# Kernel tuning notes

Measured on AMD Instinct MI355X. Metric: run time of the kernel, lower is better.

The kernel has to match this reference:

```python
import jax, jax.numpy as jnp
import numpy as np

N = 100_000   # active voxels
CIN = 64
COUT = 64
K = 3
L = 128       # voxel grid extent per axis
C = K // 2    # kernel center


def _offsets():
    # spatial offsets (z, y, x) for all non-center kernel taps, in the same
    # enumeration order as the original module's triple loop
    offs = []
    for dz in range(K):
        for dy in range(K):
            for dx in range(K):
                if (dz, dy, dx) != (C, C, C):
                    offs.append((dz - C, dy - C, dx - C))
    return offs


def _build_neighbor_map(coords):
    # coords: [N,3] int, unique. For each offset build (out_idx, in_idx) pairs
    # where voxel out_idx has an active neighbor in_idx at coords+offset.
    keys = (coords[:, 0].astype(np.int64) * L + coords[:, 1]) * L + coords[:, 2]
    order = np.argsort(keys)
    skeys = keys[order]
    pairs = []
    for (z, y, x) in _offsets():
        nb = coords + np.array([z, y, x], dtype=coords.dtype)
        valid = np.all((nb >= 0) & (nb < L), axis=1)
        nkeys = (nb[:, 0].astype(np.int64) * L + nb[:, 1]) * L + nb[:, 2]
        pos = np.clip(np.searchsorted(skeys, nkeys), 0, N - 1)
        found = valid & (skeys[pos] == nkeys)
        out_idx = np.nonzero(found)[0].astype(np.int32)
        in_idx = order[pos[found]].astype(np.int32)
        pairs.append((out_idx, in_idx))
    P = max(len(o) for o, _ in pairs)
    nei = np.zeros((len(pairs), P, 2), dtype=np.int32)
    sizes = np.zeros(len(pairs), dtype=np.int32)
    for i, (o, j) in enumerate(pairs):
        nei[i, :len(o), 0] = o
        nei[i, :len(o), 1] = j
        sizes[i] = len(o)
    return nei, sizes


def setup_inputs() -> dict:
    rng = np.random.default_rng(0)
    flat = rng.choice(L * L * L, size=N, replace=False)  # unique voxel coords
    coords = np.stack([flat // (L * L), (flat // L) % L, flat % L], axis=1).astype(np.int32)
    nei, sizes = _build_neighbor_map(coords)
    key = jax.random.key(0)
    k1, k2, k3 = jax.random.split(key, 3)
    sp_values = jax.random.normal(k1, (N, CIN), dtype=jnp.float32)
    weight = jax.random.normal(k2, (COUT, K, K, K, CIN), dtype=jnp.float32) * 0.05
    bias = jax.random.normal(k3, (COUT,), dtype=jnp.float32)
    return {"sp_values": sp_values, "weight": weight, "bias": bias,
            "nei_indices": jnp.asarray(nei), "nei_sizes": jnp.asarray(sizes)}


def reference(sp_values, weight, bias, nei_indices, nei_sizes):
    # weight: [Cout,kz,ky,kx,Cin] -> [kz,ky,kx,Cin,Cout] (matches torch permute)
    w = jnp.transpose(weight, (1, 2, 3, 4, 0))
    out = sp_values @ w[C, C, C]                                   # center tap: [N,Cout]
    offs = _offsets()
    w_offs = jnp.stack([w[z + C, y + C, x + C] for (z, y, x) in offs])  # [O,Cin,Cout]
    P = nei_indices.shape[1]
    valid = (jnp.arange(P)[None, :] < nei_sizes[:, None]).astype(sp_values.dtype)  # [O,P]
    gathered = sp_values[nei_indices[:, :, 1]] * valid[:, :, None]  # [O,P,Cin], padded rows zeroed
    contrib = jnp.einsum('opc,ocd->opd', gathered, w_offs)          # [O,P,Cout]
    out = out.at[nei_indices[:, :, 0].reshape(-1)].add(contrib.reshape(-1, out.shape[1]))
    return out + bias
```

## Files before the change

kernel.cpp:

```cpp
#include <hip/hip_runtime.h>


typedef __bf16 bf16x8 __attribute__((ext_vector_type(8)));
typedef float f32x4 __attribute__((ext_vector_type(4)));

#define LDSP 72

__device__ __forceinline__ unsigned short f2bf(float f) {
    union { float f; unsigned int u; } v; v.f = f;
    unsigned int u = v.u;
    return (unsigned short)((u + 0x7FFFu + ((u >> 16) & 1u)) >> 16);
}

__device__ __forceinline__ ushort4 cvt4(float4 v) {
    ushort4 b;
    b.x = f2bf(v.x); b.y = f2bf(v.y); b.z = f2bf(v.z); b.w = f2bf(v.w);
    return b;
}

__global__ __launch_bounds__(256) void sp3d_prep(
    const float* __restrict__ sp, const float* __restrict__ w,
    unsigned short* __restrict__ spb, unsigned short* __restrict__ wb,
    int* __restrict__ tbl, int n_rows)
{
    const long gt = (long)blockIdx.x * 256 + threadIdx.x;
    const long stride = (long)gridDim.x * 256;

    const long ntbl = 26L * n_rows;
    for (long i = gt; i < (ntbl >> 2); i += stride)
        *(int4*)&tbl[i * 4] = make_int4(-1, -1, -1, -1);
    if (gt < (ntbl & 3)) tbl[(ntbl & ~3L) + gt] = -1;

    const long nsp = (long)n_rows * 16;
    for (long i = gt; i < nsp; i += stride) {
        float4 v = *(const float4*)&sp[i * 4];
        *(ushort4*)&spb[i * 4] = cvt4(v);
    }

    for (long i = gt; i < 27 * 1024; i += stride) {
        int tp = (int)(i >> 10);
        int r  = (int)(i & 1023);
        int n = r >> 4, k4 = r & 15;
        float4 v = *(const float4*)&w[n * 1728 + tp * 64 + k4 * 4];
        *(ushort4*)&wb[(tp * 64 + n) * 64 + k4 * 4] = cvt4(v);
    }
}

__global__ __launch_bounds__(256) void sp3d_build(
    const int* __restrict__ nei, const int* __restrict__ sizes,
    int* __restrict__ tbl, int n_rows, int P)
{
    const int o = blockIdx.y;
    const int p = blockIdx.x * 256 + threadIdx.x;
    if (p < sizes[o]) {
        int2 pr = *(const int2*)&nei[(o * P + p) * 2];
        tbl[(long)o * n_rows + pr.x] = pr.y;
    }
}

__global__ __launch_bounds__(256) void sp3d_main(
    const unsigned short* __restrict__ spb, const unsigned short* __restrict__ wb,
    const float* __restrict__ bias, const int* __restrict__ tbl,
    float* __restrict__ out, int n_rows)
{
    __shared__ unsigned short Bt[2][64 * LDSP];
    __shared__ int tl[26][256];

    const int t = threadIdx.x;
    const int row0 = blockIdx.x * 256;
    const int wid = t >> 6, lane = t & 63, ml = lane & 15, quad = lane >> 4;

    {
        int r = row0 + t;
        if (r >= n_rows) r = n_rows - 1;
        #pragma unroll
        for (int o = 0; o < 26; ++o)
            tl[o][t] = tbl[(long)o * n_rows + r];
    }
    {
        int c = t;
        *(bf16x8*)&Bt[0][(c >> 3) * LDSP + (c & 7) * 8] = *(const bf16x8*)(wb + c * 8);
        c = t + 256;
        *(bf16x8*)&Bt[0][(c >> 3) * LDSP + (c & 7) * 8] = *(const bf16x8*)(wb + c * 8);
    }

    f32x4 acc[4][4];
    #pragma unroll
    for (int mg = 0; mg < 4; ++mg)
        #pragma unroll
        for (int nt = 0; nt < 4; ++nt) acc[mg][nt] = f32x4{0.f, 0.f, 0.f, 0.f};

    __syncthreads();

    int cur = 0;
    for (int tp = 0; tp < 27; ++tp) {
        bf16x8 b0[4], b1[4];
        #pragma unroll
        for (int nt = 0; nt < 4; ++nt) {
            b0[nt] = *(const bf16x8*)&Bt[cur][(nt * 16 + ml) * LDSP + quad * 8];
            b1[nt] = *(const bf16x8*)&Bt[cur][(nt * 16 + ml) * LDSP + 32 + quad * 8];
        }

        bf16x8 s0, s1;
        if (tp < 26) {
            const unsigned short* src = wb + (tp + 1) * 4096;
            s0 = *(const bf16x8*)(src + t * 8);
            s1 = *(const bf16x8*)(src + (t + 256) * 8);
        }

        int inr[4];
        #pragma unroll
        for (int mg = 0; mg < 4; ++mg) {
            int rl = wid * 64 + mg * 16 + ml;
            if (tp == 13) {
                int r = row0 + rl;
                inr[mg] = (r < n_rows) ? r : n_rows - 1;
            } else {
                int o = tp - (tp > 13 ? 1 : 0);
                inr[mg] = tl[o][rl];
            }
        }

        #pragma unroll
        for (int mg = 0; mg < 4; ++mg) {
            if (__any(inr[mg] >= 0)) {
                bf16x8 a0, a1;
                #pragma unroll
                for (int j = 0; j < 8; ++j) { a0[j] = (__bf16)0.f; a1[j] = (__bf16)0.f; }
                if (inr[mg] >= 0) {
                    const unsigned short* ap = spb + (long)inr[mg] * 64 + quad * 8;
                    a0 = *(const bf16x8*)ap;
                    a1 = *(const bf16x8*)(ap + 32);
                }
                #pragma unroll
                for (int nt = 0; nt < 4; ++nt) {
                    acc[mg][nt] = __builtin_amdgcn_mfma_f32_16x16x32_bf16(a0, b0[nt], acc[mg][nt], 0, 0, 0);
                    acc[mg][nt] = __builtin_amdgcn_mfma_f32_16x16x32_bf16(a1, b1[nt], acc[mg][nt], 0, 0, 0);
                }
            }
        }

        if (tp < 26) {
            int c = t;
            *(bf16x8*)&Bt[cur ^ 1][(c >> 3) * LDSP + (c & 7) * 8] = s0;
            c = t + 256;
            *(bf16x8*)&Bt[cur ^ 1][(c >> 3) * LDSP + (c & 7) * 8] = s1;
        }
        __syncthreads();
        cur ^= 1;
    }

    float bv[4];
    #pragma unroll
    for (int nt = 0; nt < 4; ++nt) bv[nt] = bias[nt * 16 + ml];
    #pragma unroll
    for (int mg = 0; mg < 4; ++mg) {
        int rb = row0 + wid * 64 + mg * 16 + quad * 4;
        #pragma unroll
        for (int nt = 0; nt < 4; ++nt) {
            int col = nt * 16 + ml;
            #pragma unroll
            for (int rg = 0; rg < 4; ++rg) {
                int row = rb + rg;
                if (row < n_rows) out[(long)row * 64 + col] = acc[mg][nt][rg] + bv[nt];
            }
        }
    }
}

extern "C" void kernel_launch(void* const* d_in, const int* in_sizes, int n_in,
                              void* d_out, int out_size, void* d_ws, size_t ws_size,
                              hipStream_t stream) {
    const float* sp    = (const float*)d_in[0];
    const float* w     = (const float*)d_in[1];
    const float* bias  = (const float*)d_in[2];
    const int*   nei   = (const int*)d_in[3];
    const int*   sizes = (const int*)d_in[4];
    float* out = (float*)d_out;

    const int N = in_sizes[0] / 64;
    const int P = in_sizes[3] / (26 * 2);

    char* ws = (char*)d_ws;
    unsigned short* spb = (unsigned short*)ws;
    size_t off = ((size_t)N * 64 * 2 + 255) & ~(size_t)255;
    unsigned short* wb = (unsigned short*)(ws + off);
    off = (off + 27 * 64 * 64 * 2 + 255) & ~(size_t)255;
    int* tbl = (int*)(ws + off);

    sp3d_prep<<<dim3(1024), 256, 0, stream>>>(sp, w, spb, wb, tbl, N);
    sp3d_build<<<dim3((P + 255) / 256, 26), 256, 0, stream>>>(nei, sizes, tbl, N, P);
    sp3d_main<<<dim3((N + 255) / 256), 256, 0, stream>>>(spb, wb, bias, tbl, out, N);
}
```

Before: 140.3 us.

## Prefetch next-tap gathered rows and pre-swizzle weights into MFMA fragment layout

Result: faster. 133.0 us (-5.3%).

```diff
diff --git a/kernel.cpp b/kernel.cpp
--- a/kernel.cpp
+++ b/kernel.cpp
@@ -3,8 +3,6 @@
 
 typedef __bf16 bf16x8 __attribute__((ext_vector_type(8)));
 typedef float f32x4 __attribute__((ext_vector_type(4)));
-
-#define LDSP 72
 
 __device__ __forceinline__ unsigned short f2bf(float f) {
     union { float f; unsigned int u; } v; v.f = f;
@@ -37,12 +35,16 @@
         *(ushort4*)&spb[i * 4] = cvt4(v);
     }
 
-    for (long i = gt; i < 27 * 1024; i += stride) {
-        int tp = (int)(i >> 10);
-        int r  = (int)(i & 1023);
-        int n = r >> 4, k4 = r & 15;
-        float4 v = *(const float4*)&w[n * 1728 + tp * 64 + k4 * 4];
-        *(ushort4*)&wb[(tp * 64 + n) * 64 + k4 * 4] = cvt4(v);
+    for (long i = gt; i < 27 * 512; i += stride) {
+        int tap = (int)(i >> 9);
+        int rem = (int)(i & 511);
+        int fragid = rem >> 6, lane = rem & 63;
+        int nt = fragid >> 1, half = fragid & 1, ml = lane & 15, quad = lane >> 4;
+        const float* src = w + (nt * 16 + ml) * 1728 + tap * 64 + half * 32 + quad * 8;
+        float4 v0 = *(const float4*)src;
+        float4 v1 = *(const float4*)(src + 4);
+        *(ushort4*)&wb[i * 8]     = cvt4(v0);
+        *(ushort4*)&wb[i * 8 + 4] = cvt4(v1);
     }
 }
 
@@ -58,112 +60,90 @@
     }
 }
 
-__global__ __launch_bounds__(256) void sp3d_main(
+__global__ __launch_bounds__(512) void sp3d_main(
     const unsigned short* __restrict__ spb, const unsigned short* __restrict__ wb,
     const float* __restrict__ bias, const int* __restrict__ tbl,
     float* __restrict__ out, int n_rows)
 {
-    __shared__ unsigned short Bt[2][64 * LDSP];
-    __shared__ int tl[26][256];
+    __shared__ unsigned short Bt[2][4096];
+    __shared__ int tl[26 * 128];
 
     const int t = threadIdx.x;
-    const int row0 = blockIdx.x * 256;
+    const int row0 = blockIdx.x * 128;
     const int wid = t >> 6, lane = t & 63, ml = lane & 15, quad = lane >> 4;
 
-    {
-        int r = row0 + t;
-        if (r >= n_rows) r = n_rows - 1;
-        #pragma unroll
-        for (int o = 0; o < 26; ++o)
-            tl[o][t] = tbl[(long)o * n_rows + r];
+    for (int i = t; i < 26 * 128; i += 512) {
+        int o = i >> 7;
+        int r = row0 + (i & 127);
+        tl[i] = tbl[(long)o * n_rows + (r < n_rows ? r : n_rows - 1)];
     }
-    {
-        int c = t;
-        *(bf16x8*)&Bt[0][(c >> 3) * LDSP + (c & 7) * 8] = *(const bf16x8*)(wb + c * 8);
-        c = t + 256;
-        *(bf16x8*)&Bt[0][(c >> 3) * LDSP + (c & 7) * 8] = *(const bf16x8*)(wb + c * 8);
+    *(bf16x8*)&Bt[0][t * 8] = *(const bf16x8*)(wb + t * 8);
+
+    bf16x8 z8;
+    #pragma unroll
+    for (int j = 0; j < 8; ++j) z8[j] = (__bf16)0.f;
+
+    int curv = tl[wid * 16 + ml];
+    bf16x8 a0 = z8, a1 = z8;
+    if (curv >= 0) {
+        const unsigned short* ap = spb + (long)curv * 64 + quad * 8;
+        a0 = *(const bf16x8*)ap;
+        a1 = *(const bf16x8*)(ap + 32);
     }
 
-    f32x4 acc[4][4];
+    f32x4 acc[4];
     #pragma unroll
-    for (int mg = 0; mg < 4; ++mg)
-        #pragma unroll
-        for (int nt = 0; nt < 4; ++nt) acc[mg][nt] = f32x4{0.f, 0.f, 0.f, 0.f};
+    for (int nt = 0; nt < 4; ++nt) acc[nt] = f32x4{0.f, 0.f, 0.f, 0.f};
 
     __syncthreads();
 
     int cur = 0;
     for (int tp = 0; tp < 27; ++tp) {
-        bf16x8 b0[4], b1[4];
-        #pragma unroll
-        for (int nt = 0; nt < 4; ++nt) {
-            b0[nt] = *(const bf16x8*)&Bt[cur][(nt * 16 + ml) * LDSP + quad * 8];
-            b1[nt] = *(const bf16x8*)&Bt[cur][(nt * 16 + ml) * LDSP + 32 + quad * 8];
-        }
+        bf16x8 s0 = z8;
+        if (tp < 26) s0 = *(const bf16x8*)(wb + (tp + 1) * 4096 + t * 8);
 
-        bf16x8 s0, s1;
+        int ninr = -1;
+        bf16x8 na0 = z8, na1 = z8;
         if (tp < 26) {
-            const unsigned short* src = wb + (tp + 1) * 4096;
-            s0 = *(const bf16x8*)(src + t * 8);
-            s1 = *(const bf16x8*)(src + (t + 256) * 8);
-        }
-
-        int inr[4];
-        #pragma unroll
-        for (int mg = 0; mg < 4; ++mg) {
-            int rl = wid * 64 + mg * 16 + ml;
-            if (tp == 13) {
-                int r = row0 + rl;
-                inr[mg] = (r < n_rows) ? r : n_rows - 1;
+            int tn = tp + 1;
+            if (tn == 13) {
+                int r = row0 + wid * 16 + ml;
+                ninr = (r < n_rows) ? r : n_rows - 1;
             } else {
-                int o = tp - (tp > 13 ? 1 : 0);
-                inr[mg] = tl[o][rl];
+                int o = tn - (tn > 13 ? 1 : 0);
+                ninr = tl[o * 128 + wid * 16 + ml];
+            }
+            if (ninr >= 0) {
+                const unsigned short* ap = spb + (long)ninr * 64 + quad * 8;
+                na0 = *(const bf16x8*)ap;
+                na1 = *(const bf16x8*)(ap + 32);
             }
         }
 
-        #pragma unroll
-        for (int mg = 0; mg < 4; ++mg) {
-            if (__any(inr[mg] >= 0)) {
-                bf16x8 a0, a1;
-                #pragma unroll
-                for (int j = 0; j < 8; ++j) { a0[j] = (__bf16)0.f; a1[j] = (__bf16)0.f; }
-                if (inr[mg] >= 0) {
-                    const unsigned short* ap = spb + (long)inr[mg] * 64 + quad * 8;
-                    a0 = *(const bf16x8*)ap;
-                    a1 = *(const bf16x8*)(ap + 32);
-                }
-                #pragma unroll
-                for (int nt = 0; nt < 4; ++nt) {
-                    acc[mg][nt] = __builtin_amdgcn_mfma_f32_16x16x32_bf16(a0, b0[nt], acc[mg][nt], 0, 0, 0);
-                    acc[mg][nt] = __builtin_amdgcn_mfma_f32_16x16x32_bf16(a1, b1[nt], acc[mg][nt], 0, 0, 0);
-                }
+        if (__any(curv >= 0)) {
+            #pragma unroll
+            for (int nt = 0; nt < 4; ++nt) {
+                bf16x8 b0 = *(const bf16x8*)&Bt[cur][(nt * 2 + 0) * 512 + lane * 8];
+                bf16x8 b1 = *(const bf16x8*)&Bt[cur][(nt * 2 + 1) * 512 + lane * 8];
+                acc[nt] = __builtin_amdgcn_mfma_f32_16x16x32_bf16(a0, b0, acc[nt], 0, 0, 0);
+                acc[nt] = __builtin_amdgcn_mfma_f32_16x16x32_bf16(a1, b1, acc[nt], 0, 0, 0);
             }
         }
 
-        if (tp < 26) {
-            int c = t;
-            *(bf16x8*)&Bt[cur ^ 1][(c >> 3) * LDSP + (c & 7) * 8] = s0;
-            c = t + 256;
-            *(bf16x8*)&Bt[cur ^ 1][(c >> 3) * LDSP + (c & 7) * 8] = s1;
-        }
+        if (tp < 26) *(bf16x8*)&Bt[cur ^ 1][t * 8] = s0;
         __syncthreads();
+        a0 = na0; a1 = na1; curv = ninr;
         cur ^= 1;
     }
 
-    float bv[4];
     #pragma unroll
-    for (int nt = 0; nt < 4; ++nt) bv[nt] = bias[nt * 16 + ml];
-    #pragma unroll
-    for (int mg = 0; mg < 4; ++mg) {
-        int rb = row0 + wid * 64 + mg * 16 + quad * 4;
+    for (int nt = 0; nt < 4; ++nt) {
+        int col = nt * 16 + ml;
+        float bv = bias[col];
         #pragma unroll
-        for (int nt = 0; nt < 4; ++nt) {
-            int col = nt * 16 + ml;
-            #pragma unroll
-            for (int rg = 0; rg < 4; ++rg) {
-                int row = rb + rg;
-                if (row < n_rows) out[(long)row * 64 + col] = acc[mg][nt][rg] + bv[nt];
-            }
+        for (int rg = 0; rg < 4; ++rg) {
+            int row = row0 + wid * 16 + quad * 4 + rg;
+            if (row < n_rows) out[(long)row * 64 + col] = acc[nt][rg] + bv;
         }
     }
 }
@@ -185,10 +165,10 @@
     unsigned short* spb = (unsigned short*)ws;
     size_t off = ((size_t)N * 64 * 2 + 255) & ~(size_t)255;
     unsigned short* wb = (unsigned short*)(ws + off);
-    off = (off + 27 * 64 * 64 * 2 + 255) & ~(size_t)255;
+    off = (off + 27 * 4096 * 2 + 255) & ~(size_t)255;
     int* tbl = (int*)(ws + off);
 
-    sp3d_prep<<<dim3(1024), 256, 0, stream>>>(sp, w, spb, wb, tbl, N);
+    sp3d_prep<<<dim3(2048), 256, 0, stream>>>(sp, w, spb, wb, tbl, N);
     sp3d_build<<<dim3((P + 255) / 256, 26), 256, 0, stream>>>(nei, sizes, tbl, N, P);
-    sp3d_main<<<dim3((N + 255) / 256), 256, 0, stream>>>(spb, wb, bias, tbl, out, N);
+    sp3d_main<<<dim3((N + 127) / 128), 512, 0, stream>>>(spb, wb, bias, tbl, out, N);
 }
```
